# Performance work log

Hardware: AMD Instinct MI355X
Metric: run time of the kernel (lower is better)

## Reference

```python
import jax, jax.numpy as jnp
import numpy as np

DIM = 1024
MAXLEN = 2048
EPS = 1e-6


def rms_norm(x, w):
    rms = jnp.sqrt(jnp.mean(x * x, axis=-1, keepdims=True) + EPS)
    return x / rms * w


def setup_inputs() -> dict:
    key = jax.random.key(0)
    ks = jax.random.split(key, 12)
    d = DIM
    s = 0.02
    inp = {
        "x": jax.random.normal(ks[0], (8, 2048, d), dtype=jnp.float32),
        "attn_norm_w": jnp.ones((d,), jnp.float32),
        "mlp_norm_w": jnp.ones((d,), jnp.float32),
        "wq": jax.random.normal(ks[1], (d, d), jnp.float32) * s,
        "bq": jnp.zeros((d,), jnp.float32),
        "wk": jax.random.normal(ks[2], (d, d), jnp.float32) * s,
        "bk": jnp.zeros((d,), jnp.float32),
        "wv": jax.random.normal(ks[3], (d, d), jnp.float32) * s,
        "bv": jnp.zeros((d,), jnp.float32),
        "wo": jax.random.normal(ks[4], (d, d), jnp.float32) * s,
        "bo": jnp.zeros((d,), jnp.float32),
        "w1": jax.random.normal(ks[5], (d, 4 * d), jnp.float32) * s,
        "b1": jnp.zeros((4 * d,), jnp.float32),
        "w2": jax.random.normal(ks[6], (4 * d, d), jnp.float32) * s,
        "b2": jnp.zeros((d,), jnp.float32),
    }
    return inp


def reference(x, attn_norm_w, mlp_norm_w, wq, bq, wk, bk, wv, bv, wo, bo, w1, b1, w2, b2):
    b, t, d = x.shape
    xn = rms_norm(x, attn_norm_w)
    q = xn @ wq + bq
    k = xn @ wk + bk
    v = xn @ wv + bv
    # single-head attention over full dim, scaled by sqrt(d)
    scores = jnp.einsum("btd,bsd->bts", q, k) / jnp.sqrt(jnp.asarray(d, x.dtype))
    causal = jnp.tril(jnp.ones((t, t), dtype=bool))
    scores = jnp.where(causal, scores, jnp.asarray(-1e9, x.dtype))
    probs = jax.nn.softmax(scores, axis=-1)
    attn = jnp.einsum("bts,bsd->btd", probs, v)
    x = x + attn @ wo + bo
    h = rms_norm(x, mlp_norm_w)
    x = x + jax.nn.gelu(h @ w1 + b1, approximate=False) @ w2 + b2
    return x
```

## Files before the change

### kernel.cpp

```cpp
#include <hip/hip_runtime.h>
#include <hip/hip_bf16.h>

typedef __bf16 bf16;
typedef __bf16 bf16x8 __attribute__((ext_vector_type(8)));
typedef __bf16 bf16x4 __attribute__((ext_vector_type(4)));
typedef float  f32x4  __attribute__((ext_vector_type(4)));

#define DIM   1024
#define SEQ   2048
#define BATCH 8
#define NROWS (BATCH * SEQ)
#define HID   4096

__device__ __forceinline__ void async_ld16(const bf16* g, bf16* l) {
    __builtin_amdgcn_global_load_lds(
        (__attribute__((address_space(1))) void*)(g),
        (__attribute__((address_space(3))) void*)(l),
        16, 0, 0);
}

__device__ __forceinline__ f32x4 mfma16(bf16x8 a, bf16x8 b, f32x4 c) {
    return __builtin_amdgcn_mfma_f32_16x16x32_bf16(a, b, c, 0, 0, 0);
}

template<int OUTF32, int BIASMODE, int RESID, int GELU, int SCORE, int PV>
__global__ __launch_bounds__(256) void gemm_kernel(
    const bf16* __restrict__ A, size_t aB,
    const bf16* __restrict__ B, size_t bB,
    void* __restrict__ Cv, size_t cB,
    const float* __restrict__ bias,
    const float* __restrict__ resid,
    int M, int N, int K, float scale)
{
    __shared__ alignas(16) bf16 As[128 * 64];
    __shared__ alignas(16) bf16 Bs[128 * 64];

    const int m0 = blockIdx.y * 128;
    const int n0 = blockIdx.x * 128;
    if (SCORE && n0 >= m0 + 128) return;

    const int z = blockIdx.z;
    A += (size_t)z * aB;
    B += (size_t)z * bB;

    const int t    = threadIdx.x;
    const int lane = t & 63;
    const int wave = t >> 6;
    const int wm   = wave & 1;
    const int wn   = wave >> 1;

    const int kEnd   = PV ? (m0 + 128) : K;
    const int kIters = kEnd >> 6;

    f32x4 acc[4][4] = {};

    const int srow = wave * 8 + (lane >> 3);
    const int scol = (((lane & 7) ^ ((lane >> 3) & 7)) * 8);
    const bf16* gA = A + (size_t)(m0 + srow) * (size_t)K + scol;
    const bf16* gB = B + (size_t)(n0 + srow) * (size_t)K + scol;
    bf16* lA = As + wave * 8 * 64;
    bf16* lB = Bs + wave * 8 * 64;
    const size_t r32 = (size_t)32 * (size_t)K;

    const int frow = lane & 15;
    const int cs   = (lane >> 4) ^ (frow & 7);
    const bf16* pa0 = As + (wm * 64 + frow) * 64 + cs * 8;
    const bf16* pa1 = As + (wm * 64 + frow) * 64 + (cs ^ 4) * 8;
    const bf16* pb0 = Bs + (wn * 64 + frow) * 64 + cs * 8;
    const bf16* pb1 = Bs + (wn * 64 + frow) * 64 + (cs ^ 4) * 8;

    for (int kt = 0; kt < kIters; ++kt) {
        #pragma unroll
        for (int j = 0; j < 4; ++j) {
            async_ld16(gA + j * r32, lA + j * 32 * 64);
            async_ld16(gB + j * r32, lB + j * 32 * 64);
        }
        gA += 64; gB += 64;
        __syncthreads();

        {
            bf16x8 af[4], bg[4];
            #pragma unroll
            for (int i = 0; i < 4; ++i) af[i] = *(const bf16x8*)(pa0 + i * 16 * 64);
            #pragma unroll
            for (int j = 0; j < 4; ++j) bg[j] = *(const bf16x8*)(pb0 + j * 16 * 64);
            #pragma unroll
            for (int i = 0; i < 4; ++i)
                #pragma unroll
                for (int j = 0; j < 4; ++j)
                    acc[i][j] = mfma16(af[i], bg[j], acc[i][j]);
        }
        {
            bf16x8 af[4], bg[4];
            #pragma unroll
            for (int i = 0; i < 4; ++i) af[i] = *(const bf16x8*)(pa1 + i * 16 * 64);
            #pragma unroll
            for (int j = 0; j < 4; ++j) bg[j] = *(const bf16x8*)(pb1 + j * 16 * 64);
            #pragma unroll
            for (int i = 0; i < 4; ++i)
                #pragma unroll
                for (int j = 0; j < 4; ++j)
                    acc[i][j] = mfma16(af[i], bg[j], acc[i][j]);
        }
        __syncthreads();
    }

    const int col  = lane & 15;
    const int row4 = (lane >> 4) * 4;
    const size_t cOff = (size_t)z * cB;
    #pragma unroll
    for (int i = 0; i < 4; ++i) {
        const int mBase = m0 + wm * 64 + i * 16 + row4;
        #pragma unroll
        for (int j = 0; j < 4; ++j) {
            const int n = n0 + wn * 64 + j * 16 + col;
            const float bcol = (BIASMODE == 1) ? bias[n] : 0.0f;
            #pragma unroll
            for (int r = 0; r < 4; ++r) {
                const int m = mBase + r;
                float v = acc[i][j][r];
                if (BIASMODE == 1) v += bcol;
                if (BIASMODE == 2) v += bias[m];
                if (SCORE) { v *= scale; if (n > m) v = -1e30f; }
                if (GELU)  { v = 0.5f * v * (1.0f + erff(v * 0.70710678118654752f)); }
                const size_t idx = cOff + (size_t)m * (size_t)N + (size_t)n;
                if (RESID) v += resid[idx];
                if (OUTF32) ((float*)Cv)[idx] = v;
                else        ((bf16*)Cv)[idx]  = (bf16)v;
            }
        }
    }
}

__global__ __launch_bounds__(256) void rmsnorm_kernel(
    const float* __restrict__ x, const float* __restrict__ w, bf16* __restrict__ out)
{
    const int row = blockIdx.x;
    const int t   = threadIdx.x;
    const float4 v = ((const float4*)(x + (size_t)row * DIM))[t];
    float ss = v.x * v.x + v.y * v.y + v.z * v.z + v.w * v.w;
    #pragma unroll
    for (int off = 32; off; off >>= 1) ss += __shfl_down(ss, off);
    __shared__ float part[4];
    if ((t & 63) == 0) part[t >> 6] = ss;
    __syncthreads();
    const float tot  = part[0] + part[1] + part[2] + part[3];
    const float rinv = rsqrtf(tot * (1.0f / DIM) + 1e-6f);
    const float4 wv = ((const float4*)w)[t];
    bf16x4 o;
    o[0] = (bf16)(v.x * rinv * wv.x);
    o[1] = (bf16)(v.y * rinv * wv.y);
    o[2] = (bf16)(v.z * rinv * wv.z);
    o[3] = (bf16)(v.w * rinv * wv.w);
    *(bf16x4*)(out + (size_t)row * DIM + t * 4) = o;
}

__global__ __launch_bounds__(256) void transpose_w_kernel(
    const float* __restrict__ src, bf16* __restrict__ dst, int R, int C)
{
    __shared__ float tile[32][33];
    const int tx = threadIdx.x & 31;
    const int ty = threadIdx.x >> 5;
    const int c0 = blockIdx.x * 32;
    const int r0 = blockIdx.y * 32;
    #pragma unroll
    for (int j = 0; j < 32; j += 8)
        tile[ty + j][tx] = src[(size_t)(r0 + ty + j) * C + c0 + tx];
    __syncthreads();
    #pragma unroll
    for (int j = 0; j < 32; j += 8)
        dst[(size_t)(c0 + ty + j) * R + r0 + tx] = (bf16)tile[tx][ty + j];
}

__global__ __launch_bounds__(256) void softmax_kernel(bf16* __restrict__ S)
{
    const int t = blockIdx.x;
    const int b = blockIdx.y;
    bf16* p = S + ((size_t)b * SEQ + t) * SEQ;
    const int send = ((t >> 7) + 1) << 7;
    const int tid  = threadIdx.x;
    const int lane = tid & 63;
    const int wave = tid >> 6;

    float v[8];
    int cnt = 0;
    float m = -3.0e38f;
    for (int i = tid; i < send; i += 256) { const float f = (float)p[i]; v[cnt++] = f; m = fmaxf(m, f); }
    #pragma unroll
    for (int off = 32; off; off >>= 1) m = fmaxf(m, __shfl_down(m, off));
    __shared__ float red[4];
    if (lane == 0) red[wave] = m;
    __syncthreads();
    m = fmaxf(fmaxf(red[0], red[1]), fmaxf(red[2], red[3]));
    __syncthreads();

    float s = 0.0f;
    for (int k2 = 0; k2 < cnt; ++k2) { v[k2] = __expf(v[k2] - m); s += v[k2]; }
    #pragma unroll
    for (int off = 32; off; off >>= 1) s += __shfl_down(s, off);
    if (lane == 0) red[wave] = s;
    __syncthreads();
    s = red[0] + red[1] + red[2] + red[3];
    const float inv = 1.0f / s;
    cnt = 0;
    for (int i = tid; i < send; i += 256) p[i] = (bf16)(v[cnt++] * inv);
}

extern "C" void kernel_launch(void* const* d_in, const int* in_sizes, int n_in,
                              void* d_out, int out_size, void* d_ws, size_t ws_size,
                              hipStream_t stream)
{
    const float* x   = (const float*)d_in[0];
    const float* anw = (const float*)d_in[1];
    const float* mnw = (const float*)d_in[2];
    const float* wq  = (const float*)d_in[3];
    const float* bq  = (const float*)d_in[4];
    const float* wk  = (const float*)d_in[5];
    const float* bk  = (const float*)d_in[6];
    const float* wv  = (const float*)d_in[7];
    const float* bv  = (const float*)d_in[8];
    const float* wo  = (const float*)d_in[9];
    const float* bo  = (const float*)d_in[10];
    const float* w1  = (const float*)d_in[11];
    const float* b1  = (const float*)d_in[12];
    const float* w2  = (const float*)d_in[13];
    const float* b2  = (const float*)d_in[14];
    float* out = (float*)d_out;

    char* ws = (char*)d_ws;
    const size_t MB = 1024 * 1024;
    bf16* wqT = (bf16*)(ws + 0 * MB);
    bf16* wkT = (bf16*)(ws + 2 * MB);
    bf16* wvT = (bf16*)(ws + 4 * MB);
    bf16* woT = (bf16*)(ws + 6 * MB);
    bf16* w1T = (bf16*)(ws + 8 * MB);
    bf16* w2T = (bf16*)(ws + 16 * MB);
    bf16* xn  = (bf16*)(ws + 24 * MB);
    bf16* q   = (bf16*)(ws + 56 * MB);
    bf16* k   = (bf16*)(ws + 88 * MB);
    bf16* vT  = (bf16*)(ws + 120 * MB);
    bf16* S   = (bf16*)(ws + 152 * MB);
    bf16* attn = xn;
    bf16* h    = q;
    bf16* mid  = k;

    const dim3 blk(256);

    transpose_w_kernel<<<dim3(DIM / 32, DIM / 32), blk, 0, stream>>>(wq, wqT, DIM, DIM);
    transpose_w_kernel<<<dim3(DIM / 32, DIM / 32), blk, 0, stream>>>(wk, wkT, DIM, DIM);
    transpose_w_kernel<<<dim3(DIM / 32, DIM / 32), blk, 0, stream>>>(wv, wvT, DIM, DIM);
    transpose_w_kernel<<<dim3(DIM / 32, DIM / 32), blk, 0, stream>>>(wo, woT, DIM, DIM);
    transpose_w_kernel<<<dim3(HID / 32, DIM / 32), blk, 0, stream>>>(w1, w1T, DIM, HID);
    transpose_w_kernel<<<dim3(DIM / 32, HID / 32), blk, 0, stream>>>(w2, w2T, HID, DIM);

    rmsnorm_kernel<<<NROWS, blk, 0, stream>>>(x, anw, xn);

    gemm_kernel<0, 1, 0, 0, 0, 0><<<dim3(DIM / 128, NROWS / 128, 1), blk, 0, stream>>>(
        xn, 0, wqT, 0, q, 0, bq, nullptr, NROWS, DIM, DIM, 1.0f);
    gemm_kernel<0, 1, 0, 0, 0, 0><<<dim3(DIM / 128, NROWS / 128, 1), blk, 0, stream>>>(
        xn, 0, wkT, 0, k, 0, bk, nullptr, NROWS, DIM, DIM, 1.0f);
    gemm_kernel<0, 2, 0, 0, 0, 0><<<dim3(SEQ / 128, DIM / 128, BATCH), blk, 0, stream>>>(
        wvT, 0, xn, (size_t)SEQ * DIM, vT, (size_t)DIM * SEQ, bv, nullptr, DIM, SEQ, DIM, 1.0f);

    gemm_kernel<0, 0, 0, 0, 1, 0><<<dim3(SEQ / 128, SEQ / 128, BATCH), blk, 0, stream>>>(
        q, (size_t)SEQ * DIM, k, (size_t)SEQ * DIM, S, (size_t)SEQ * SEQ,
        nullptr, nullptr, SEQ, SEQ, DIM, 0.03125f);

    softmax_kernel<<<dim3(SEQ, BATCH), blk, 0, stream>>>(S);

    gemm_kernel<0, 0, 0, 0, 0, 1><<<dim3(DIM / 128, SEQ / 128, BATCH), blk, 0, stream>>>(
        S, (size_t)SEQ * SEQ, vT, (size_t)DIM * SEQ, attn, (size_t)SEQ * DIM,
        nullptr, nullptr, SEQ, DIM, SEQ, 1.0f);

    gemm_kernel<1, 1, 1, 0, 0, 0><<<dim3(DIM / 128, NROWS / 128, 1), blk, 0, stream>>>(
        attn, 0, woT, 0, out, 0, bo, x, NROWS, DIM, DIM, 1.0f);

    rmsnorm_kernel<<<NROWS, blk, 0, stream>>>(out, mnw, h);

    gemm_kernel<0, 1, 0, 1, 0, 0><<<dim3(HID / 128, NROWS / 128, 1), blk, 0, stream>>>(
        h, 0, w1T, 0, mid, 0, b1, nullptr, NROWS, HID, DIM, 1.0f);

    gemm_kernel<1, 1, 1, 0, 0, 0><<<dim3(DIM / 128, NROWS / 128, 1), blk, 0, stream>>>(
        mid, 0, w2T, 0, out, 0, b2, out, NROWS, DIM, HID, 1.0f);
}
```

Before: 972.1 us.

## Fuse Q/K projections, use tanh GELU, vectorize softmax row access

Merges the Q and K projection GEMMs into one GEMM with N=2*DIM. To support this, leading-dimension parameters are added to the GEMM kernel and the transposed weights and biases are packed next to each other. Replaces the erf GELU in the W1 epilogue with a tanh approximation built on fast exp and reciprocal, which is cheaper but numerically different from exact GELU. Rewrites the softmax so each thread loads and stores eight bf16 values as one vector instead of using strided scalar accesses.

Result: no change. 984.4 us (+1.3%).

```diff
diff --git a/kernel.cpp b/kernel.cpp
--- a/kernel.cpp
+++ b/kernel.cpp
@@ -25,9 +25,9 @@
 
 template<int OUTF32, int BIASMODE, int RESID, int GELU, int SCORE, int PV>
 __global__ __launch_bounds__(256) void gemm_kernel(
-    const bf16* __restrict__ A, size_t aB,
-    const bf16* __restrict__ B, size_t bB,
-    void* __restrict__ Cv, size_t cB,
+    const bf16* __restrict__ A, size_t aB, int lda,
+    const bf16* __restrict__ B, size_t bB, int ldb,
+    void* __restrict__ Cv, size_t cB, int ldc,
     const float* __restrict__ bias,
     const float* __restrict__ resid,
     int M, int N, int K, float scale)
@@ -56,11 +56,12 @@
 
     const int srow = wave * 8 + (lane >> 3);
     const int scol = (((lane & 7) ^ ((lane >> 3) & 7)) * 8);
-    const bf16* gA = A + (size_t)(m0 + srow) * (size_t)K + scol;
-    const bf16* gB = B + (size_t)(n0 + srow) * (size_t)K + scol;
+    const bf16* gA = A + (size_t)(m0 + srow) * (size_t)lda + scol;
+    const bf16* gB = B + (size_t)(n0 + srow) * (size_t)ldb + scol;
     bf16* lA = As + wave * 8 * 64;
     bf16* lB = Bs + wave * 8 * 64;
-    const size_t r32 = (size_t)32 * (size_t)K;
+    const size_t r32A = (size_t)32 * (size_t)lda;
+    const size_t r32B = (size_t)32 * (size_t)ldb;
 
     const int frow = lane & 15;
     const int cs   = (lane >> 4) ^ (frow & 7);
@@ -72,8 +73,8 @@
     for (int kt = 0; kt < kIters; ++kt) {
         #pragma unroll
         for (int j = 0; j < 4; ++j) {
-            async_ld16(gA + j * r32, lA + j * 32 * 64);
-            async_ld16(gB + j * r32, lB + j * 32 * 64);
+            async_ld16(gA + j * r32A, lA + j * 32 * 64);
+            async_ld16(gB + j * r32B, lB + j * 32 * 64);
         }
         gA += 64; gB += 64;
         __syncthreads();
@@ -122,8 +123,13 @@
                 if (BIASMODE == 1) v += bcol;
                 if (BIASMODE == 2) v += bias[m];
                 if (SCORE) { v *= scale; if (n > m) v = -1e30f; }
-                if (GELU)  { v = 0.5f * v * (1.0f + erff(v * 0.70710678118654752f)); }
-                const size_t idx = cOff + (size_t)m * (size_t)N + (size_t)n;
+                if (GELU) {
+                    const float u  = v * (0.7978845608f + 0.0356774081f * v * v);
+                    const float e  = __expf(2.0f * u);
+                    const float th = 1.0f - 2.0f * __builtin_amdgcn_rcpf(e + 1.0f);
+                    v = 0.5f * v * (1.0f + th);
+                }
+                const size_t idx = cOff + (size_t)m * (size_t)ldc + (size_t)n;
                 if (RESID) v += resid[idx];
                 if (OUTF32) ((float*)Cv)[idx] = v;
                 else        ((bf16*)Cv)[idx]  = (bf16)v;
@@ -183,9 +189,13 @@
     const int wave = tid >> 6;
 
     float v[8];
-    int cnt = 0;
     float m = -3.0e38f;
-    for (int i = tid; i < send; i += 256) { const float f = (float)p[i]; v[cnt++] = f; m = fmaxf(m, f); }
+    const bool act = (tid * 8) < send;
+    if (act) {
+        const bf16x8 x8 = *(const bf16x8*)(p + tid * 8);
+        #pragma unroll
+        for (int i = 0; i < 8; ++i) { v[i] = (float)x8[i]; m = fmaxf(m, v[i]); }
+    }
     #pragma unroll
     for (int off = 32; off; off >>= 1) m = fmaxf(m, __shfl_down(m, off));
     __shared__ float red[4];
@@ -195,15 +205,22 @@
     __syncthreads();
 
     float s = 0.0f;
-    for (int k2 = 0; k2 < cnt; ++k2) { v[k2] = __expf(v[k2] - m); s += v[k2]; }
+    if (act) {
+        #pragma unroll
+        for (int i = 0; i < 8; ++i) { v[i] = __expf(v[i] - m); s += v[i]; }
+    }
     #pragma unroll
     for (int off = 32; off; off >>= 1) s += __shfl_down(s, off);
     if (lane == 0) red[wave] = s;
     __syncthreads();
     s = red[0] + red[1] + red[2] + red[3];
     const float inv = 1.0f / s;
-    cnt = 0;
-    for (int i = tid; i < send; i += 256) p[i] = (bf16)(v[cnt++] * inv);
+    if (act) {
+        bf16x8 o;
+        #pragma unroll
+        for (int i = 0; i < 8; ++i) o[i] = (bf16)(v[i] * inv);
+        *(bf16x8*)(p + tid * 8) = o;
+    }
 }
 
 extern "C" void kernel_launch(void* const* d_in, const int* in_sizes, int n_in,
@@ -229,25 +246,27 @@
 
     char* ws = (char*)d_ws;
     const size_t MB = 1024 * 1024;
-    bf16* wqT = (bf16*)(ws + 0 * MB);
-    bf16* wkT = (bf16*)(ws + 2 * MB);
-    bf16* wvT = (bf16*)(ws + 4 * MB);
-    bf16* woT = (bf16*)(ws + 6 * MB);
-    bf16* w1T = (bf16*)(ws + 8 * MB);
-    bf16* w2T = (bf16*)(ws + 16 * MB);
-    bf16* xn  = (bf16*)(ws + 24 * MB);
-    bf16* q   = (bf16*)(ws + 56 * MB);
-    bf16* k   = (bf16*)(ws + 88 * MB);
-    bf16* vT  = (bf16*)(ws + 120 * MB);
-    bf16* S   = (bf16*)(ws + 152 * MB);
+    bf16* wqkT = (bf16*)(ws + 0 * MB);
+    bf16* wvT  = (bf16*)(ws + 4 * MB);
+    bf16* woT  = (bf16*)(ws + 6 * MB);
+    bf16* w1T  = (bf16*)(ws + 8 * MB);
+    bf16* w2T  = (bf16*)(ws + 16 * MB);
+    bf16* xn   = (bf16*)(ws + 24 * MB);
+    bf16* qk   = (bf16*)(ws + 56 * MB);
+    bf16* vT   = (bf16*)(ws + 120 * MB);
+    bf16* S    = (bf16*)(ws + 152 * MB);
+    float* bqk = (float*)(ws + 152 * MB);
     bf16* attn = xn;
-    bf16* h    = q;
-    bf16* mid  = k;
+    bf16* h    = qk;
+    bf16* mid  = (bf16*)(ws + 88 * MB);
 
     const dim3 blk(256);
 
-    transpose_w_kernel<<<dim3(DIM / 32, DIM / 32), blk, 0, stream>>>(wq, wqT, DIM, DIM);
-    transpose_w_kernel<<<dim3(DIM / 32, DIM / 32), blk, 0, stream>>>(wk, wkT, DIM, DIM);
+    hipMemcpyAsync(bqk,        bq, DIM * sizeof(float), hipMemcpyDeviceToDevice, stream);
+    hipMemcpyAsync(bqk + DIM,  bk, DIM * sizeof(float), hipMemcpyDeviceToDevice, stream);
+
+    transpose_w_kernel<<<dim3(DIM / 32, DIM / 32), blk, 0, stream>>>(wq, wqkT, DIM, DIM);
+    transpose_w_kernel<<<dim3(DIM / 32, DIM / 32), blk, 0, stream>>>(wk, wqkT + (size_t)DIM * DIM, DIM, DIM);
     transpose_w_kernel<<<dim3(DIM / 32, DIM / 32), blk, 0, stream>>>(wv, wvT, DIM, DIM);
     transpose_w_kernel<<<dim3(DIM / 32, DIM / 32), blk, 0, stream>>>(wo, woT, DIM, DIM);
     transpose_w_kernel<<<dim3(HID / 32, DIM / 32), blk, 0, stream>>>(w1, w1T, DIM, HID);
@@ -255,31 +274,31 @@
 
     rmsnorm_kernel<<<NROWS, blk, 0, stream>>>(x, anw, xn);
 
-    gemm_kernel<0, 1, 0, 0, 0, 0><<<dim3(DIM / 128, NROWS / 128, 1), blk, 0, stream>>>(
-        xn, 0, wqT, 0, q, 0, bq, nullptr, NROWS, DIM, DIM, 1.0f);
-    gemm_kernel<0, 1, 0, 0, 0, 0><<<dim3(DIM / 128, NROWS / 128, 1), blk, 0, stream>>>(
-        xn, 0, wkT, 0, k, 0, bk, nullptr, NROWS, DIM, DIM, 1.0f);
+    gemm_kernel<0, 1, 0, 0, 0, 0><<<dim3(2 * DIM / 128, NROWS / 128, 1), blk, 0, stream>>>(
+        xn, 0, DIM, wqkT, 0, DIM, qk, 0, 2 * DIM, bqk, nullptr, NROWS, 2 * DIM, DIM, 1.0f);
+
     gemm_kernel<0, 2, 0, 0, 0, 0><<<dim3(SEQ / 128, DIM / 128, BATCH), blk, 0, stream>>>(
-        wvT, 0, xn, (size_t)SEQ * DIM, vT, (size_t)DIM * SEQ, bv, nullptr, DIM, SEQ, DIM, 1.0f);
+        wvT, 0, DIM, xn, (size_t)SEQ * DIM, DIM, vT, (size_t)DIM * SEQ, SEQ,
+        bv, nullptr, DIM, SEQ, DIM, 1.0f);
 
     gemm_kernel<0, 0, 0, 0, 1, 0><<<dim3(SEQ / 128, SEQ / 128, BATCH), blk, 0, stream>>>(
-        q, (size_t)SEQ * DIM, k, (size_t)SEQ * DIM, S, (size_t)SEQ * SEQ,
-        nullptr, nullptr, SEQ, SEQ, DIM, 0.03125f);
+        qk, (size_t)SEQ * 2 * DIM, 2 * DIM, qk + DIM, (size_t)SEQ * 2 * DIM, 2 * DIM,
+        S, (size_t)SEQ * SEQ, SEQ, nullptr, nullptr, SEQ, SEQ, DIM, 0.03125f);
 
     softmax_kernel<<<dim3(SEQ, BATCH), blk, 0, stream>>>(S);
 
     gemm_kernel<0, 0, 0, 0, 0, 1><<<dim3(DIM / 128, SEQ / 128, BATCH), blk, 0, stream>>>(
-        S, (size_t)SEQ * SEQ, vT, (size_t)DIM * SEQ, attn, (size_t)SEQ * DIM,
+        S, (size_t)SEQ * SEQ, SEQ, vT, (size_t)DIM * SEQ, SEQ, attn, (size_t)SEQ * DIM, DIM,
         nullptr, nullptr, SEQ, DIM, SEQ, 1.0f);
 
     gemm_kernel<1, 1, 1, 0, 0, 0><<<dim3(DIM / 128, NROWS / 128, 1), blk, 0, stream>>>(
-        attn, 0, woT, 0, out, 0, bo, x, NROWS, DIM, DIM, 1.0f);
+        attn, 0, DIM, woT, 0, DIM, out, 0, DIM, bo, x, NROWS, DIM, DIM, 1.0f);
 
     rmsnorm_kernel<<<NROWS, blk, 0, stream>>>(out, mnw, h);
 
     gemm_kernel<0, 1, 0, 1, 0, 0><<<dim3(HID / 128, NROWS / 128, 1), blk, 0, stream>>>(
-        h, 0, w1T, 0, mid, 0, b1, nullptr, NROWS, HID, DIM, 1.0f);
+        h, 0, DIM, w1T, 0, DIM, mid, 0, HID, b1, nullptr, NROWS, HID, DIM, 1.0f);
 
     gemm_kernel<1, 1, 1, 0, 0, 0><<<dim3(DIM / 128, NROWS / 128, 1), blk, 0, stream>>>(
-        mid, 0, w2T, 0, out, 0, b2, out, NROWS, DIM, HID, 1.0f);
-}
+        mid, 0, HID, w2T, 0, HID, out, 0, DIM, b2, out, NROWS, DIM, HID, 1.0f);
+}
```
